# Optimization experiments

Measured on AMD Instinct MI355X. Metric: run time of the kernel, lower is better.

## Reference

```python
import jax, jax.numpy as jnp
import numpy as np
from jax import lax

B, C, H, W = 128, 256, 32, 32
KH, KW = 8, 8


def depthwise_xcorr(x, kernel):
    """Depthwise cross-correlation: each (batch, channel) plane of x is
    correlated with the matching (batch, channel) plane of kernel,
    equivalent to F.conv2d(x.view(1,B*C,H,W), k.view(B*C,1,kh,kw), groups=B*C).
    Note torch conv2d is cross-correlation (no kernel flip), matching lax."""
    b, c, h, w = x.shape
    kh, kw = kernel.shape[2], kernel.shape[3]
    xr = x.reshape(1, b * c, h, w)
    kr = kernel.reshape(b * c, 1, kh, kw)
    out = lax.conv_general_dilated(
        xr, kr,
        window_strides=(1, 1),
        padding='VALID',
        dimension_numbers=('NCHW', 'OIHW', 'NCHW'),
        feature_group_count=b * c,
    )  # (1, b*c, h-kh+1, w-kw+1)
    return out.reshape(b, c, h - kh + 1, w - kw + 1)


def setup_inputs() -> dict:
    key = jax.random.key(0)
    k1, k2 = jax.random.split(key)
    x = jax.random.normal(k1, (B, C, H, W), dtype=jnp.float32)
    kernel = jax.random.normal(k2, (B, C, KH, KW), dtype=jnp.float32)
    weight = jnp.ones((3,), dtype=jnp.float32)  # nn.Parameter(torch.ones(channels))
    return {"x": x, "kernel": kernel, "weight": weight}


def reference(x, kernel, weight):
    # Original runs three identical depthwise-correlation implementations
    # (testCon2dSvf, testCon2dPSvf, F.conv2d) over the same data, then blends
    # with softmax weights. Since all three compute the same correlation,
    # out = (w0 + w1 + w2) * corr. We compute the correlation once.
    corr = depthwise_xcorr(x, kernel)
    w = jax.nn.softmax(weight, axis=0)
    return (w[0] + w[1] + w[2]) * corr
```

## Files before the change

kernel.cpp:

```cpp
#include <hip/hip_runtime.h>


#define NPLANES (128 * 256)
#define PPB 4
#define RST 20
#define XROWS 40
#define XP (XROWS * RST)
#define TAPB (PPB * XP)
#define TKY 48
#define TPP (8 * TKY)
#define LDS_DW (TAPB + PPB * TPP)
#define OH 25
#define OW 25

typedef __attribute__((ext_vector_type(8))) short short8;
typedef __attribute__((ext_vector_type(4))) float f32x4;
typedef __attribute__((ext_vector_type(4))) unsigned uint4v;

__device__ __forceinline__ unsigned cvt_pk_bf16(float a, float b) {
    unsigned r;
    asm("v_cvt_pk_bf16_f32 %0, %1, %2" : "=v"(r) : "v"(a), "v"(b));
    return r;
}

__global__ __launch_bounds__(256)
void dwxcorr_kernel(const float* __restrict__ x,
                    const float* __restrict__ kern,
                    float* __restrict__ out) {
    __shared__ unsigned ldsu[LDS_DW];
    const int tid  = threadIdx.x;
    const int wave = tid >> 6;
    const int l    = tid & 63;
    const int plane = blockIdx.x * PPB + wave;

    {
        const int row  = l >> 1;
        const int half = l & 1;
        const float* g = x + (size_t)plane * 1024 + row * 32 + half * 16;
        const float4 v0 = *reinterpret_cast<const float4*>(g + 0);
        const float4 v1 = *reinterpret_cast<const float4*>(g + 4);
        const float4 v2 = *reinterpret_cast<const float4*>(g + 8);
        const float4 v3 = *reinterpret_cast<const float4*>(g + 12);
        uint4v w;
        unsigned* base = &ldsu[wave * XP + row * RST + half * 8];
        w.x = cvt_pk_bf16(v0.x, v0.y); w.y = cvt_pk_bf16(v0.z, v0.w);
        w.z = cvt_pk_bf16(v1.x, v1.y); w.w = cvt_pk_bf16(v1.z, v1.w);
        *reinterpret_cast<uint4v*>(base + 0) = w;
        w.x = cvt_pk_bf16(v2.x, v2.y); w.y = cvt_pk_bf16(v2.z, v2.w);
        w.z = cvt_pk_bf16(v3.x, v3.y); w.w = cvt_pk_bf16(v3.z, v3.w);
        *reinterpret_cast<uint4v*>(base + 4) = w;
    }

    const int tb0 = TAPB + wave * TPP;
    {
        const uint4v z4 = {0u, 0u, 0u, 0u};
        *reinterpret_cast<uint4v*>(&ldsu[tb0 + 4 * l]) = z4;
        *reinterpret_cast<uint2*>(&ldsu[tb0 + 256 + 2 * l]) =
            make_uint2(0u, 0u);
    }
    if (l < 24) {
        const int ky = l / 3;
        const int q  = l - 3 * ky;
        const float* g = kern + (size_t)plane * 64 + ky * 8;
        const float4 v0 = *reinterpret_cast<const float4*>(g + 0);
        const float4 v1 = *reinterpret_cast<const float4*>(g + 4);
        uint4v m;
        int off;
        if (q == 0) {
            m.x = cvt_pk_bf16(v0.x, v0.y); m.y = cvt_pk_bf16(v0.z, v0.w);
            m.z = cvt_pk_bf16(v1.x, v1.y); m.w = cvt_pk_bf16(v1.z, v1.w);
            off = 8;
        } else if (q == 1) {
            m.x = 0u; m.y = 0u; m.z = 0u;
            m.w = cvt_pk_bf16(0.f, v0.x);
            off = 28;
        } else {
            m.x = cvt_pk_bf16(v0.y, v0.z); m.y = cvt_pk_bf16(v0.w, v1.x);
            m.z = cvt_pk_bf16(v1.y, v1.z); m.w = cvt_pk_bf16(v1.w, 0.f);
            off = 32;
        }
        *reinterpret_cast<uint4v*>(&ldsu[tb0 + ky * TKY + off]) = m;
    }

    asm volatile("s_waitcnt lgkmcnt(0)" ::: "memory");
    __builtin_amdgcn_sched_barrier(0);

    const int c = l & 15;
    const int a = l >> 4;

    const unsigned* xb = &ldsu[wave * XP + 4 * a];
    const unsigned* tb = &ldsu[tb0];

    int off0, off1;
    {
        int s = 8 * a - c;
        int st = (s >> 1) + 8;
        st = st < 0 ? 0 : (st > 20 ? 20 : st);
        off0 = (s & 1) * 24 + st;
        s = 8 * a - 16 - c;
        st = (s >> 1) + 8;
        st = st < 0 ? 0 : (st > 20 ? 20 : st);
        off1 = (s & 1) * 24 + st;
    }

    f32x4 acc00 = {0.f, 0.f, 0.f, 0.f};
    f32x4 acc01 = {0.f, 0.f, 0.f, 0.f};
    f32x4 acc10 = {0.f, 0.f, 0.f, 0.f};
    f32x4 acc11 = {0.f, 0.f, 0.f, 0.f};

#pragma unroll
    for (int ky = 0; ky < 8; ++ky) {
        const short8 a0 =
            *reinterpret_cast<const short8*>(xb + (ky + c) * RST);
        const short8 a1 =
            *reinterpret_cast<const short8*>(xb + (16 + ky + c) * RST);
        const unsigned* bp = tb + ky * TKY;
        uint4v bu0, bu1;
        bu0.x = bp[off0 + 0]; bu0.y = bp[off0 + 1];
        bu0.z = bp[off0 + 2]; bu0.w = bp[off0 + 3];
        bu1.x = bp[off1 + 0]; bu1.y = bp[off1 + 1];
        bu1.z = bp[off1 + 2]; bu1.w = bp[off1 + 3];
        const short8 b0 = __builtin_bit_cast(short8, bu0);
        const short8 b1 = __builtin_bit_cast(short8, bu1);
        acc00 = __builtin_amdgcn_mfma_f32_16x16x32_bf16(a0, b0, acc00, 0, 0, 0);
        acc01 = __builtin_amdgcn_mfma_f32_16x16x32_bf16(a0, b1, acc01, 0, 0, 0);
        acc10 = __builtin_amdgcn_mfma_f32_16x16x32_bf16(a1, b0, acc10, 0, 0, 0);
        acc11 = __builtin_amdgcn_mfma_f32_16x16x32_bf16(a1, b1, acc11, 0, 0, 0);
    }

    float* op = out + (size_t)plane * (OH * OW);
#pragma unroll
    for (int reg = 0; reg < 4; ++reg) {
        const int r0 = 4 * a + reg;
        op[r0 * OW + c] = acc00[reg];
        if (c <= 8) op[r0 * OW + 16 + c] = acc01[reg];
        if (r0 <= 8) {
            op[(16 + r0) * OW + c] = acc10[reg];
            if (c <= 8) op[(16 + r0) * OW + 16 + c] = acc11[reg];
        }
    }
}

extern "C" void kernel_launch(void* const* d_in, const int* in_sizes, int n_in,
                              void* d_out, int out_size, void* d_ws, size_t ws_size,
                              hipStream_t stream) {
    const float* x = (const float*)d_in[0];
    const float* k = (const float*)d_in[1];
    float* out = (float*)d_out;
    const int nblocks = NPLANES / PPB;
    dwxcorr_kernel<<<nblocks, 256, 0, stream>>>(x, k, out);
}
```

Measured before the change: 39.96 us.

## Process two planes per wave with prefetch of second plane during compute

Each wave now handles two planes instead of one, halving the block count. The global loads for the second plane's input and taps are issued before the first plane's MFMA compute, so memory latency overlaps with compute. The second plane then reuses the same LDS region after the first plane finishes. This adds register pressure from holding the prefetched data and halves the number of blocks in flight, in a kernel that is likely already near memory-bandwidth bound.

Measured after the change: 40.72 us. No clear change (+1.9%).

```diff
diff --git a/kernel.cpp b/kernel.cpp
--- a/kernel.cpp
+++ b/kernel.cpp
@@ -2,14 +2,14 @@
 
 
 #define NPLANES (128 * 256)
-#define PPB 4
+#define PPB 8
 #define RST 20
 #define XROWS 40
 #define XP (XROWS * RST)
-#define TAPB (PPB * XP)
+#define TAPB (4 * XP)
 #define TKY 48
 #define TPP (8 * TKY)
-#define LDS_DW (TAPB + PPB * TPP)
+#define LDS_DW (TAPB + 4 * TPP)
 #define OH 25
 #define OW 25
 
@@ -23,91 +23,44 @@
     return r;
 }
 
-__global__ __launch_bounds__(256)
-void dwxcorr_kernel(const float* __restrict__ x,
-                    const float* __restrict__ kern,
-                    float* __restrict__ out) {
-    __shared__ unsigned ldsu[LDS_DW];
-    const int tid  = threadIdx.x;
-    const int wave = tid >> 6;
-    const int l    = tid & 63;
-    const int plane = blockIdx.x * PPB + wave;
+__device__ __forceinline__ void write_x(unsigned* xbase,
+                                        const float4& v0, const float4& v1,
+                                        const float4& v2, const float4& v3) {
+    uint4v w;
+    w.x = cvt_pk_bf16(v0.x, v0.y); w.y = cvt_pk_bf16(v0.z, v0.w);
+    w.z = cvt_pk_bf16(v1.x, v1.y); w.w = cvt_pk_bf16(v1.z, v1.w);
+    *reinterpret_cast<uint4v*>(xbase + 0) = w;
+    w.x = cvt_pk_bf16(v2.x, v2.y); w.y = cvt_pk_bf16(v2.z, v2.w);
+    w.z = cvt_pk_bf16(v3.x, v3.y); w.w = cvt_pk_bf16(v3.z, v3.w);
+    *reinterpret_cast<uint4v*>(xbase + 4) = w;
+}
+__device__ __forceinline__ void write_taps(unsigned* ldsu, int tb0, int ky, int q,
+                                           const float4& v0, const float4& v1) {
+    uint4v m;
+    int off;
+    if (q == 0) {
+        m.x = cvt_pk_bf16(v0.x, v0.y); m.y = cvt_pk_bf16(v0.z, v0.w);
+        m.z = cvt_pk_bf16(v1.x, v1.y); m.w = cvt_pk_bf16(v1.z, v1.w);
+        off = 8;
+    } else if (q == 1) {
+        m.x = 0u; m.y = 0u; m.z = 0u;
+        m.w = cvt_pk_bf16(0.f, v0.x);
+        off = 28;
+    } else {
+        m.x = cvt_pk_bf16(v0.y, v0.z); m.y = cvt_pk_bf16(v0.w, v1.x);
+        m.z = cvt_pk_bf16(v1.y, v1.z); m.w = cvt_pk_bf16(v1.w, 0.f);
+        off = 32;
+    }
+    *reinterpret_cast<uint4v*>(&ldsu[tb0 + ky * TKY + off]) = m;
+}
 
-    {
-        const int row  = l >> 1;
-        const int half = l & 1;
-        const float* g = x + (size_t)plane * 1024 + row * 32 + half * 16;
-        const float4 v0 = *reinterpret_cast<const float4*>(g + 0);
-        const float4 v1 = *reinterpret_cast<const float4*>(g + 4);
-        const float4 v2 = *reinterpret_cast<const float4*>(g + 8);
-        const float4 v3 = *reinterpret_cast<const float4*>(g + 12);
-        uint4v w;
-        unsigned* base = &ldsu[wave * XP + row * RST + half * 8];
-        w.x = cvt_pk_bf16(v0.x, v0.y); w.y = cvt_pk_bf16(v0.z, v0.w);
-        w.z = cvt_pk_bf16(v1.x, v1.y); w.w = cvt_pk_bf16(v1.z, v1.w);
-        *reinterpret_cast<uint4v*>(base + 0) = w;
-        w.x = cvt_pk_bf16(v2.x, v2.y); w.y = cvt_pk_bf16(v2.z, v2.w);
-        w.z = cvt_pk_bf16(v3.x, v3.y); w.w = cvt_pk_bf16(v3.z, v3.w);
-        *reinterpret_cast<uint4v*>(base + 4) = w;
-    }
-
-    const int tb0 = TAPB + wave * TPP;
-    {
-        const uint4v z4 = {0u, 0u, 0u, 0u};
-        *reinterpret_cast<uint4v*>(&ldsu[tb0 + 4 * l]) = z4;
-        *reinterpret_cast<uint2*>(&ldsu[tb0 + 256 + 2 * l]) =
-            make_uint2(0u, 0u);
-    }
-    if (l < 24) {
-        const int ky = l / 3;
-        const int q  = l - 3 * ky;
-        const float* g = kern + (size_t)plane * 64 + ky * 8;
-        const float4 v0 = *reinterpret_cast<const float4*>(g + 0);
-        const float4 v1 = *reinterpret_cast<const float4*>(g + 4);
-        uint4v m;
-        int off;
-        if (q == 0) {
-            m.x = cvt_pk_bf16(v0.x, v0.y); m.y = cvt_pk_bf16(v0.z, v0.w);
-            m.z = cvt_pk_bf16(v1.x, v1.y); m.w = cvt_pk_bf16(v1.z, v1.w);
-            off = 8;
-        } else if (q == 1) {
-            m.x = 0u; m.y = 0u; m.z = 0u;
-            m.w = cvt_pk_bf16(0.f, v0.x);
-            off = 28;
-        } else {
-            m.x = cvt_pk_bf16(v0.y, v0.z); m.y = cvt_pk_bf16(v0.w, v1.x);
-            m.z = cvt_pk_bf16(v1.y, v1.z); m.w = cvt_pk_bf16(v1.w, 0.f);
-            off = 32;
-        }
-        *reinterpret_cast<uint4v*>(&ldsu[tb0 + ky * TKY + off]) = m;
-    }
-
-    asm volatile("s_waitcnt lgkmcnt(0)" ::: "memory");
-    __builtin_amdgcn_sched_barrier(0);
-
-    const int c = l & 15;
-    const int a = l >> 4;
-
-    const unsigned* xb = &ldsu[wave * XP + 4 * a];
-    const unsigned* tb = &ldsu[tb0];
-
-    int off0, off1;
-    {
-        int s = 8 * a - c;
-        int st = (s >> 1) + 8;
-        st = st < 0 ? 0 : (st > 20 ? 20 : st);
-        off0 = (s & 1) * 24 + st;
-        s = 8 * a - 16 - c;
-        st = (s >> 1) + 8;
-        st = st < 0 ? 0 : (st > 20 ? 20 : st);
-        off1 = (s & 1) * 24 + st;
-    }
-
+__device__ __forceinline__ void compute_plane(const unsigned* xb, const unsigned* tb,
+                                              int off0, int off1, int c, int a,
+                                              float* op) {
     f32x4 acc00 = {0.f, 0.f, 0.f, 0.f};
     f32x4 acc01 = {0.f, 0.f, 0.f, 0.f};
     f32x4 acc10 = {0.f, 0.f, 0.f, 0.f};
     f32x4 acc11 = {0.f, 0.f, 0.f, 0.f};
-
 #pragma unroll
     for (int ky = 0; ky < 8; ++ky) {
         const short8 a0 =
@@ -127,8 +80,6 @@
         acc10 = __builtin_amdgcn_mfma_f32_16x16x32_bf16(a1, b0, acc10, 0, 0, 0);
         acc11 = __builtin_amdgcn_mfma_f32_16x16x32_bf16(a1, b1, acc11, 0, 0, 0);
     }
-
-    float* op = out + (size_t)plane * (OH * OW);
 #pragma unroll
     for (int reg = 0; reg < 4; ++reg) {
         const int r0 = 4 * a + reg;
@@ -141,6 +92,86 @@
     }
 }
 
+__global__ __launch_bounds__(256)
+void dwxcorr_kernel(const float* __restrict__ x,
+                    const float* __restrict__ kern,
+                    float* __restrict__ out) {
+    __shared__ unsigned ldsu[LDS_DW];
+    const int tid  = threadIdx.x;
+    const int wave = tid >> 6;
+    const int l    = tid & 63;
+    const int p0   = blockIdx.x * PPB + wave;
+    const int p1   = p0 + 4;
+
+    const int row  = l >> 1;
+    const int half = l & 1;
+    const int tky  = l / 3;
+    const int tq   = l - 3 * tky;
+
+    unsigned* xbase = &ldsu[wave * XP + row * RST + half * 8];
+    const int tb0 = TAPB + wave * TPP;
+
+    {
+        const uint4v z4 = {0u, 0u, 0u, 0u};
+        *reinterpret_cast<uint4v*>(&ldsu[tb0 + 4 * l]) = z4;
+        *reinterpret_cast<uint2*>(&ldsu[tb0 + 256 + 2 * l]) = make_uint2(0u, 0u);
+    }
+
+    const float* gx0 = x + (size_t)p0 * 1024 + row * 32 + half * 16;
+    float4 a0 = *reinterpret_cast<const float4*>(gx0 + 0);
+    float4 a1 = *reinterpret_cast<const float4*>(gx0 + 4);
+    float4 a2 = *reinterpret_cast<const float4*>(gx0 + 8);
+    float4 a3 = *reinterpret_cast<const float4*>(gx0 + 12);
+    float4 t0, t1;
+    if (l < 24) {
+        const float* gk0 = kern + (size_t)p0 * 64 + tky * 8;
+        t0 = *reinterpret_cast<const float4*>(gk0 + 0);
+        t1 = *reinterpret_cast<const float4*>(gk0 + 4);
+    }
+    write_x(xbase, a0, a1, a2, a3);
+    if (l < 24) write_taps(ldsu, tb0, tky, tq, t0, t1);
+
+    const float* gx1 = x + (size_t)p1 * 1024 + row * 32 + half * 16;
+    float4 b0 = *reinterpret_cast<const float4*>(gx1 + 0);
+    float4 b1 = *reinterpret_cast<const float4*>(gx1 + 4);
+    float4 b2 = *reinterpret_cast<const float4*>(gx1 + 8);
+    float4 b3 = *reinterpret_cast<const float4*>(gx1 + 12);
+    float4 u0, u1;
+    if (l < 24) {
+        const float* gk1 = kern + (size_t)p1 * 64 + tky * 8;
+        u0 = *reinterpret_cast<const float4*>(gk1 + 0);
+        u1 = *reinterpret_cast<const float4*>(gk1 + 4);
+    }
+
+    asm volatile("s_waitcnt lgkmcnt(0)" ::: "memory");
+    __builtin_amdgcn_sched_barrier(0);
+
+    const int c = l & 15;
+    const int a = l >> 4;
+    const unsigned* xb = &ldsu[wave * XP + 4 * a];
+    const unsigned* tb = &ldsu[tb0];
+    int off0, off1;
+    {
+        int s = 8 * a - c;
+        int st = (s >> 1) + 8;
+        st = st < 0 ? 0 : (st > 20 ? 20 : st);
+        off0 = (s & 1) * 24 + st;
+        s = 8 * a - 16 - c;
+        st = (s >> 1) + 8;
+        st = st < 0 ? 0 : (st > 20 ? 20 : st);
+        off1 = (s & 1) * 24 + st;
+    }
+    compute_plane(xb, tb, off0, off1, c, a, out + (size_t)p0 * (OH * OW));
+
+    write_x(xbase, b0, b1, b2, b3);
+    if (l < 24) write_taps(ldsu, tb0, tky, tq, u0, u1);
+
+    asm volatile("s_waitcnt lgkmcnt(0)" ::: "memory");
+    __builtin_amdgcn_sched_barrier(0);
+
+    compute_plane(xb, tb, off0, off1, c, a, out + (size_t)p1 * (OH * OW));
+}
+
 extern "C" void kernel_launch(void* const* d_in, const int* in_sizes, int n_in,
                               void* d_out, int out_size, void* d_ws, size_t ws_size,
                               hipStream_t stream) {
```
